# Kernel tuning notes

Measured on AMD Instinct MI355X. Metric: run time of the kernel, lower is better.

## Reference

```python
import jax, jax.numpy as jnp
import numpy as np

NUM_HEADS = 8
GRAPH_DIM = 64
K_RATIO = 0.1
SIM_THRESH = 0.6


def _gat_layer(h_in, mask, W, a_src, a_dst, b):
    # PyG GATConv (heads=1, eval mode): lin (no bias), alpha = LeakyReLU(a_src.h_j + a_dst.h_i),
    # softmax over source nodes j per target i (edges given by dense mask, self loops included), + bias.
    h = h_in @ W                                   # [N, F]
    asrc = h @ a_src                               # [N] source term
    adst = h @ a_dst                               # [N] target term
    logits = jax.nn.leaky_relu(adst[:, None] + asrc[None, :], 0.2)  # [target i, source j]
    logits = jnp.where(mask.T, logits, -1e30)      # mask[j,i]: edge src j -> dst i (symmetric here)
    alpha = jax.nn.softmax(logits, axis=-1)
    return alpha @ h + b


def _forward(x, w_qkv, w_proj, b_proj, gat0_W, gat0_asrc, gat0_adst, gat0_b,
             gat1_W, gat1_asrc, gat1_adst, gat1_b, w_g2a, b_g2a):
    B, C, H, W = x.shape
    HW = H * W
    nh = NUM_HEADS
    hd = C // nh
    scale = hd ** -0.5
    x_seq = x.reshape(B, C, HW).transpose(0, 2, 1)                 # [B, HW, C]

    # ---- build_spatial_graph ----
    importance = jnp.var(x_seq, axis=-1, ddof=1)                   # torch.var default unbiased
    N = int(HW * K_RATIO)                                          # 102 nodes
    _, top_idx = jax.lax.top_k(importance, N)                      # [B, N]
    feats = jnp.take_along_axis(x_seq, top_idx[..., None], axis=1) # [B, N, C]
    fn = feats / jnp.clip(jnp.linalg.norm(feats, axis=-1, keepdims=True), 1e-12)
    sim = fn @ fn.transpose(0, 2, 1)                               # [B, N, N]
    adj = sim > SIM_THRESH
    adj = adj | jnp.eye(N, dtype=bool)                             # GATConv add_self_loops

    # ---- per-batch GAT stack + graph_to_attn ----
    def per_graph(f, m):
        g = jax.nn.relu(_gat_layer(f, m, gat0_W, gat0_asrc, gat0_adst, gat0_b))
        g = jax.nn.relu(_gat_layer(g, m, gat1_W, gat1_asrc, gat1_adst, gat1_b))
        return jax.nn.sigmoid(g @ w_g2a.T + b_g2a)                 # [N, nh]
    gw = jax.vmap(per_graph)(feats, adj)                           # [B, N, nh]

    # ---- dense multi-head attention ----
    qkv = (x_seq @ w_qkv.T).reshape(B, HW, 3, nh, hd).transpose(2, 0, 3, 1, 4)
    q, k, v = qkv[0], qkv[1], qkv[2]                               # [B, nh, HW, hd]
    scores = jnp.einsum('bhqd,bhkd->bhqk', q, k) * scale           # [B, nh, HW, HW]

    # ---- graph modulation scatter (replaces the nested python loops) ----
    vals = jnp.where(adj[..., None], gw[:, :, None, :] * gw[:, None, :, :], 0.0)  # [B, N, N, nh]
    gm = jnp.zeros_like(scores)
    bidx = jnp.arange(B)[:, None, None]
    gm = gm.at[bidx, :, top_idx[:, :, None], top_idx[:, None, :]].set(vals)
    scores = scores + gm

    attn = jax.nn.softmax(scores, axis=-1)                         # dropout is identity in eval
    out = jnp.einsum('bhqk,bhkd->bhqd', attn, v).transpose(0, 2, 1, 3).reshape(B, HW, C)
    out = out @ w_proj.T + b_proj
    return out.transpose(0, 2, 1).reshape(B, C, H, W)


def setup_inputs() -> dict:
    key = jax.random.key(0)
    ks = jax.random.split(key, 16)
    dim, gd, nh = 256, GRAPH_DIM, NUM_HEADS
    B, H, W = 8, 32, 32
    s = 0.02
    return {
        'x': jax.random.normal(ks[0], (B, dim, H, W), dtype=jnp.float32),
        'w_qkv': s * jax.random.normal(ks[1], (3 * dim, dim), dtype=jnp.float32),
        'w_proj': s * jax.random.normal(ks[2], (dim, dim), dtype=jnp.float32),
        'b_proj': jnp.zeros((dim,), dtype=jnp.float32),
        'gat0_W': s * jax.random.normal(ks[3], (dim, gd), dtype=jnp.float32),
        'gat0_asrc': s * jax.random.normal(ks[4], (gd,), dtype=jnp.float32),
        'gat0_adst': s * jax.random.normal(ks[5], (gd,), dtype=jnp.float32),
        'gat0_b': jnp.zeros((gd,), dtype=jnp.float32),
        'gat1_W': s * jax.random.normal(ks[6], (gd, gd), dtype=jnp.float32),
        'gat1_asrc': s * jax.random.normal(ks[7], (gd,), dtype=jnp.float32),
        'gat1_adst': s * jax.random.normal(ks[8], (gd,), dtype=jnp.float32),
        'gat1_b': jnp.zeros((gd,), dtype=jnp.float32),
        'w_g2a': s * jax.random.normal(ks[9], (nh, gd), dtype=jnp.float32),
        'b_g2a': jnp.zeros((nh,), dtype=jnp.float32),
    }


def reference(x, w_qkv, w_proj, b_proj, gat0_W, gat0_asrc, gat0_adst, gat0_b,
              gat1_W, gat1_asrc, gat1_adst, gat1_b, w_g2a, b_g2a):
    return _forward(x, w_qkv, w_proj, b_proj, gat0_W, gat0_asrc, gat0_adst, gat0_b,
                    gat1_W, gat1_asrc, gat1_adst, gat1_b, w_g2a, b_g2a)
```

## Files before the change

kernel.cpp:

```cpp
#include <hip/hip_runtime.h>
#include <math.h>

#define NB 8
#define CDIM 256
#define HWD 1024
#define NH 8
#define HD 32
#define NN 102
#define GD 64

typedef __attribute__((ext_vector_type(8))) short bf16x8;
typedef __attribute__((ext_vector_type(4))) float f32x4;

__device__ inline short f2bf(float f) {
  union { float f; unsigned u; } v; v.f = f;
  unsigned r = v.u + 0x7fffu + ((v.u >> 16) & 1u);
  return (short)(r >> 16);
}
__device__ inline float bf2f(short s) {
  union { unsigned u; float f; } v;
  v.u = ((unsigned)(unsigned short)s) << 16;
  return v.f;
}

__global__ __launch_bounds__(256) void wsplit_k(const float* __restrict__ w_qkv,
                                                const float* __restrict__ w_proj,
                                                short* __restrict__ wqh, short* __restrict__ wql,
                                                short* __restrict__ wph, short* __restrict__ wpl) {
  int t = blockIdx.x * 256 + threadIdx.x;
  if (t < 196608) {
    float v = w_qkv[t];
    short hi = f2bf(v);
    wqh[t] = hi; wql[t] = f2bf(v - bf2f(hi));
  } else {
    int u = t - 196608;
    float v = w_proj[u];
    short hi = f2bf(v);
    wph[u] = hi; wpl[u] = f2bf(v - bf2f(hi));
  }
}

__global__ __launch_bounds__(256) void xsplit_k(const float* __restrict__ x,
                                                short* __restrict__ xth,
                                                short* __restrict__ xtl) {
  __shared__ float tile[64][65];
  int p0 = blockIdx.x * 64, c0 = blockIdx.y * 64, b = blockIdx.z;
  int t = threadIdx.x;
  {
    int g = t >> 6, p = t & 63;
#pragma unroll
    for (int i = 0; i < 16; ++i) {
      int cc = g * 16 + i;
      tile[cc][p] = x[((size_t)(b * 256 + c0 + cc)) * 1024 + p0 + p];
    }
  }
  __syncthreads();
  {
    int p = t >> 2, cs = (t & 3) * 16;
    size_t rb = ((size_t)(b * 1024 + p0 + p)) * 256 + c0 + cs;
#pragma unroll
    for (int g = 0; g < 4; ++g) {
      short4 hv, lv;
      float f0 = tile[cs + g * 4 + 0][p];
      float f1 = tile[cs + g * 4 + 1][p];
      float f2 = tile[cs + g * 4 + 2][p];
      float f3 = tile[cs + g * 4 + 3][p];
      hv.x = f2bf(f0); lv.x = f2bf(f0 - bf2f(hv.x));
      hv.y = f2bf(f1); lv.y = f2bf(f1 - bf2f(hv.y));
      hv.z = f2bf(f2); lv.z = f2bf(f2 - bf2f(hv.z));
      hv.w = f2bf(f3); lv.w = f2bf(f3 - bf2f(hv.w));
      *(short4*)(xth + rb + g * 4) = hv;
      *(short4*)(xtl + rb + g * 4) = lv;
    }
  }
}

__global__ __launch_bounds__(256) void prep_k(const float* __restrict__ g0W,
                                              const float* __restrict__ g1W,
                                              short* __restrict__ w0bT,
                                              short* __restrict__ w1bT) {
  int t = blockIdx.x * 256 + threadIdx.x;
  if (t < 16384) {
    int c = t >> 6, f = t & 63;
    w0bT[f * 256 + c] = f2bf(g0W[t]);
  } else if (t < 20480) {
    int u2 = t - 16384;
    int c = u2 >> 6, f = u2 & 63;
    w1bT[f * 64 + c] = f2bf(g1W[u2]);
  }
}

__global__ __launch_bounds__(256) void importance_k(const float* __restrict__ x,
                                                    float* __restrict__ imp) {
  __shared__ float red[8][33];
  int bp = blockIdx.x;
  int b = bp >> 5, p0 = (bp & 31) << 5;
  int t = threadIdx.x;
  int pl = t & 31, cg = t >> 5;
  const float* xp = x + (size_t)b * CDIM * HWD + p0 + pl;
  float s = 0.f;
  for (int cc = 0; cc < 32; ++cc) s += xp[(size_t)(cg * 32 + cc) * HWD];
  red[cg][pl] = s;
  __syncthreads();
  float tot = 0.f;
  for (int g = 0; g < 8; ++g) tot += red[g][pl];
  float mean = tot * (1.f / CDIM);
  __syncthreads();
  float v = 0.f;
  for (int cc = 0; cc < 32; ++cc) {
    float d = xp[(size_t)(cg * 32 + cc) * HWD] - mean;
    v += d * d;
  }
  red[cg][pl] = v;
  __syncthreads();
  if (t < 32) {
    float vv = 0.f;
    for (int g = 0; g < 8; ++g) vv += red[g][t];
    imp[b * 1024 + p0 + t] = vv * (1.f / (CDIM - 1));
  }
}

union GraphLDS {
  struct { float sv[1024]; int si[1024]; } tk;
  struct {
    short h0T[64 * 136];
    short alphaB[102 * 136];
    short gB[102 * 72];
  } m;
};

__global__ __launch_bounds__(1024) void graph_k(
    const float* __restrict__ x, const float* __restrict__ imp,
    const short* __restrict__ w0bT, const short* __restrict__ w1bT,
    const float* __restrict__ g0as, const float* __restrict__ g0ad,
    const float* __restrict__ g0b,
    const float* __restrict__ g1as, const float* __restrict__ g1ad,
    const float* __restrict__ g1b,
    const float* __restrict__ wg2a, const float* __restrict__ bg2a,
    int* __restrict__ nodeof, short* __restrict__ fnG,
    unsigned char* __restrict__ adjG, float* __restrict__ gwb) {
  __shared__ GraphLDS u;
  __shared__ ushort adjPack[NN][8];
  __shared__ float normL[NN];
  __shared__ float asrcL[NN], adstL[NN];
  __shared__ int topiL[NN];
  int b = blockIdx.x, t = threadIdx.x;
  int wv = t >> 6, lane = t & 63, quad = lane >> 4, l16 = lane & 15;

  u.tk.sv[t] = imp[b * 1024 + t];
  u.tk.si[t] = t;
  nodeof[b * 1024 + t] = -1;
  __syncthreads();
  for (int k = 2; k <= 1024; k <<= 1) {
    for (int j = k >> 1; j > 0; j >>= 1) {
      int ixj = t ^ j;
      if (ixj > t) {
        bool up = ((t & k) == 0);
        float a = u.tk.sv[t], c = u.tk.sv[ixj];
        if ((a > c) == up) {
          u.tk.sv[t] = c; u.tk.sv[ixj] = a;
          int ti = u.tk.si[t]; u.tk.si[t] = u.tk.si[ixj]; u.tk.si[ixj] = ti;
        }
      }
      __syncthreads();
    }
  }
  if (t >= 1024 - NN) {
    int n = 1023 - t;
    int idx = u.tk.si[t];
    topiL[n] = idx;
    nodeof[b * 1024 + idx] = n;
  }
  __syncthreads();

  {
    int n = t >> 3, g = t & 7;
    if (n < NN) {
      int idx = topiL[n];
      const float* xb = x + (size_t)b * CDIM * HWD + idx;
      float vbuf[32];
      float ssl = 0.f;
#pragma unroll
      for (int cc = 0; cc < 32; ++cc) {
        float v = xb[(size_t)(g * 32 + cc) * HWD];
        vbuf[cc] = v;
        ssl += v * v;
      }
      ssl += __shfl_xor(ssl, 1);
      ssl += __shfl_xor(ssl, 2);
      ssl += __shfl_xor(ssl, 4);
      float nrm = sqrtf(ssl);
      float rn = 1.f / fmaxf(nrm, 1e-12f);
      if (g == 0) normL[n] = nrm;
      short* fp = fnG + ((size_t)b * 112 + n) * 256 + g * 32;
#pragma unroll
      for (int cc = 0; cc < 32; cc += 4) {
        short4 s4 = {f2bf(vbuf[cc] * rn), f2bf(vbuf[cc + 1] * rn),
                     f2bf(vbuf[cc + 2] * rn), f2bf(vbuf[cc + 3] * rn)};
        *(short4*)(fp + cc) = s4;
      }
    }
  }
  for (int e = t; e < 64 * 34; e += 1024) {
    int f = e / 34, c = 102 + (e % 34);
    u.m.h0T[f * 136 + c] = 0;
  }
  __syncthreads();

  for (int tile = wv; tile < 49; tile += 16) {
    int I = tile / 7, J = tile % 7;
    const short* ap = fnG + ((size_t)b * 112 + I * 16 + l16) * 256 + quad * 8;
    const short* bp = fnG + ((size_t)b * 112 + J * 16 + l16) * 256 + quad * 8;
    f32x4 acc = (f32x4){0.f, 0.f, 0.f, 0.f};
#pragma unroll
    for (int kb = 0; kb < 8; ++kb)
      acc = __builtin_amdgcn_mfma_f32_16x16x32_bf16(*(const bf16x8*)(ap + kb * 32),
                                                    *(const bf16x8*)(bp + kb * 32), acc, 0, 0, 0);
#pragma unroll
    for (int r = 0; r < 4; ++r) {
      int i = I * 16 + quad * 4 + r, j = J * 16 + l16;
      bool e = (acc[r] > 0.6f) || (i == j);
      unsigned long long m = __ballot(e);
      if (l16 == 0) {
        int row = I * 16 + quad * 4 + r;
        if (row < NN) adjPack[row][J] = (ushort)((m >> (quad * 16)) & 0xFFFFull);
      }
      if (i < NN && j < NN) adjG[(size_t)b * NN * NN + i * NN + j] = e ? 1 : 0;
    }
  }
  __syncthreads();

  for (int tile = wv; tile < 28; tile += 16) {
    int mt = tile >> 2, nt = tile & 3;
    const short* ap = fnG + ((size_t)b * 112 + mt * 16 + l16) * 256 + quad * 8;
    const short* bp = w0bT + (nt * 16 + l16) * 256 + quad * 8;
    f32x4 acc = (f32x4){0.f, 0.f, 0.f, 0.f};
#pragma unroll
    for (int kb = 0; kb < 8; ++kb)
      acc = __builtin_amdgcn_mfma_f32_16x16x32_bf16(*(const bf16x8*)(ap + kb * 32),
                                                    *(const bf16x8*)(bp + kb * 32), acc, 0, 0, 0);
    int f = nt * 16 + l16;
#pragma unroll
    for (int r = 0; r < 4; ++r) {
      int node = mt * 16 + quad * 4 + r;
      if (node < NN) u.m.h0T[f * 136 + node] = f2bf(acc[r] * normL[node]);
    }
  }
  __syncthreads();

  for (int layer = 0; layer < 2; ++layer) {
    const float* avs = layer ? g1as : g0as;
    const float* avd = layer ? g1ad : g0ad;
    const float* bias = layer ? g1b : g0b;
    {
      int n = t >> 3, g = t & 7;
      if (n < NN) {
        float s1 = 0.f, s2 = 0.f;
#pragma unroll
        for (int uu = 0; uu < 8; ++uu) {
          int f = g * 8 + uu;
          float hv = bf2f(u.m.h0T[f * 136 + n]);
          s1 += hv * avs[f];
          s2 += hv * avd[f];
        }
        s1 += __shfl_xor(s1, 1); s1 += __shfl_xor(s1, 2); s1 += __shfl_xor(s1, 4);
        s2 += __shfl_xor(s2, 1); s2 += __shfl_xor(s2, 2); s2 += __shfl_xor(s2, 4);
        if (g == 0) { asrcL[n] = s1; adstL[n] = s2; }
      }
    }
    __syncthreads();
    for (int i = wv; i < NN; i += 16) {
      float zi = adstL[i];
      int j1 = 64 + lane;
      bool e0 = (adjPack[i][lane >> 4] >> (lane & 15)) & 1;
      bool e1 = (j1 < NN) && ((adjPack[i][j1 >> 4] >> (j1 & 15)) & 1);
      float p0 = 0.f, p1 = 0.f;
      if (e0) { float z = zi + asrcL[lane]; p0 = __expf(z > 0.f ? z : 0.2f * z); }
      if (e1) { float z = zi + asrcL[j1]; p1 = __expf(z > 0.f ? z : 0.2f * z); }
      float s = p0 + p1;
      s += __shfl_xor(s, 1); s += __shfl_xor(s, 2); s += __shfl_xor(s, 4);
      s += __shfl_xor(s, 8); s += __shfl_xor(s, 16); s += __shfl_xor(s, 32);
      float inv = 1.f / s;
      u.m.alphaB[i * 136 + lane] = f2bf(p0 * inv);
      u.m.alphaB[i * 136 + 64 + lane] = f2bf(p1 * inv);
    }
    __syncthreads();
    for (int tile = wv; tile < 28; tile += 16) {
      int mt = tile >> 2, nt = tile & 3;
      int ar = mt * 16 + l16; if (ar > NN - 1) ar = NN - 1;
      const short* ap = &u.m.alphaB[ar * 136 + quad * 8];
      const short* bp = &u.m.h0T[(nt * 16 + l16) * 136 + quad * 8];
      f32x4 acc = (f32x4){0.f, 0.f, 0.f, 0.f};
#pragma unroll
      for (int kb = 0; kb < 4; ++kb)
        acc = __builtin_amdgcn_mfma_f32_16x16x32_bf16(*(const bf16x8*)(ap + kb * 32),
                                                      *(const bf16x8*)(bp + kb * 32), acc, 0, 0, 0);
      int f = nt * 16 + l16;
      float bv = bias[f];
#pragma unroll
      for (int r = 0; r < 4; ++r) {
        int i = mt * 16 + quad * 4 + r;
        if (i < NN) u.m.gB[i * 72 + f] = f2bf(fmaxf(acc[r] + bv, 0.f));
      }
    }
    __syncthreads();
    if (layer == 0) {
      for (int tile = wv; tile < 28; tile += 16) {
        int mt = tile >> 2, nt = tile & 3;
        int ar = mt * 16 + l16; if (ar > NN - 1) ar = NN - 1;
        const short* ap = &u.m.gB[ar * 72 + quad * 8];
        const short* bp = w1bT + (nt * 16 + l16) * 64 + quad * 8;
        f32x4 acc = (f32x4){0.f, 0.f, 0.f, 0.f};
#pragma unroll
        for (int kb = 0; kb < 2; ++kb)
          acc = __builtin_amdgcn_mfma_f32_16x16x32_bf16(*(const bf16x8*)(ap + kb * 32),
                                                        *(const bf16x8*)(bp + kb * 32), acc, 0, 0, 0);
        int f = nt * 16 + l16;
#pragma unroll
        for (int r = 0; r < 4; ++r) {
          int node = mt * 16 + quad * 4 + r;
          if (node < NN) u.m.h0T[f * 136 + node] = f2bf(acc[r]);
        }
      }
      __syncthreads();
    }
  }
  float* wgL = (float*)&u.m.alphaB[0];
  if (t < 512) wgL[t] = wg2a[t];
  __syncthreads();
  if (t < NN * NH) {
    int n = t >> 3, h = t & 7;
    float z = bg2a[h];
#pragma unroll
    for (int c = 0; c < GD; ++c) z += bf2f(u.m.gB[n * 72 + c]) * wgL[h * 64 + c];
    gwb[((size_t)b * NN + n) * NH + h] = 1.f / (1.f + __expf(-z));
  }
}

__global__ __launch_bounds__(256, 4) void qkv_k(const short* __restrict__ xth,
                                                const short* __restrict__ xtl,
                                                const short* __restrict__ wqh,
                                                const short* __restrict__ wql,
                                                short* __restrict__ qhp, short* __restrict__ qlp,
                                                short* __restrict__ khp, short* __restrict__ klp,
                                                short* __restrict__ vtp) {
  __shared__ short vs_s[4][32 * 24];
  int t = threadIdx.x, wid = t >> 6, lane = t & 63, quad = lane >> 4, l16 = lane & 15;
  int m0 = blockIdx.x * 64, y = blockIdx.y;
  int b = m0 >> 10;
  int row = m0 + wid * 16 + l16;
  int p_base = (m0 & 1023) + wid * 16;
  int qi = y >> 3, n0 = (y & 7) * 32;
  const short* wh = wqh + ((size_t)qi * 256 + n0) * 256;
  const short* wl = wql + ((size_t)qi * 256 + n0) * 256;
  const short* arh = xth + (size_t)row * 256 + quad * 8;
  const short* arl = xtl + (size_t)row * 256 + quad * 8;
  f32x4 acc[2];
  acc[0] = (f32x4){0.f, 0.f, 0.f, 0.f};
  acc[1] = (f32x4){0.f, 0.f, 0.f, 0.f};
#pragma unroll
  for (int kb = 0; kb < 8; ++kb) {
    bf16x8 ah = *(const bf16x8*)(arh + kb * 32);
    bf16x8 al = *(const bf16x8*)(arl + kb * 32);
#pragma unroll
    for (int nt = 0; nt < 2; ++nt) {
      size_t wo = (size_t)(nt * 16 + l16) * 256 + kb * 32 + quad * 8;
      bf16x8 bh_ = *(const bf16x8*)(wh + wo);
      bf16x8 bl_ = *(const bf16x8*)(wl + wo);
      acc[nt] = __builtin_amdgcn_mfma_f32_16x16x32_bf16(ah, bh_, acc[nt], 0, 0, 0);
      acc[nt] = __builtin_amdgcn_mfma_f32_16x16x32_bf16(ah, bl_, acc[nt], 0, 0, 0);
      acc[nt] = __builtin_amdgcn_mfma_f32_16x16x32_bf16(al, bh_, acc[nt], 0, 0, 0);
    }
  }
  if (qi < 2) {
    const float scale = (qi == 0) ? 0.17677669529663687f : 1.f;
    short* hp = (qi == 0) ? qhp : khp;
    short* lp = (qi == 0) ? qlp : klp;
#pragma unroll
    for (int nt = 0; nt < 2; ++nt) {
      int nq = n0 + nt * 16 + l16;
      int h = nq >> 5, d = nq & 31;
#pragma unroll
      for (int r = 0; r < 4; ++r) {
        int p = p_base + quad * 4 + r;
        float v = acc[nt][r] * scale;
        short hi = f2bf(v);
        short lo = f2bf(v - bf2f(hi));
        size_t e = ((size_t)(b * 8 + h) * 1024 + p) * 32 + d;
        hp[e] = hi;
        lp[e] = lo;
      }
    }
  } else {
    short* vs = &vs_s[wid][0];
#pragma unroll
    for (int nt = 0; nt < 2; ++nt)
#pragma unroll
      for (int r = 0; r < 4; ++r)
        vs[(nt * 16 + l16) * 24 + quad * 4 + r] = f2bf(acc[nt][r]);
    int cl = lane >> 1, hf = lane & 1;
    int nq = n0 + cl;
    int h = nq >> 5, d = nq & 31;
    size_t rb = ((size_t)(b * 8 + h) * 32 + d) * 1024 + p_base + hf * 8;
    *(bf16x8*)(vtp + rb) = *(const bf16x8*)(vs + cl * 24 + hf * 8);
  }
}

__global__ __launch_bounds__(256, 4) void attn_k(const short* __restrict__ qh,
                                                 const short* __restrict__ ql,
                                                 const short* __restrict__ kh,
                                                 const short* __restrict__ kl,
                                                 const short* __restrict__ vt,
                                                 const int* __restrict__ nodeof,
                                                 const float* __restrict__ gw,
                                                 const unsigned char* __restrict__ adj,
                                                 float* __restrict__ po,
                                                 float* __restrict__ pl) {
  __shared__ __align__(16) short p_s[4][16 * 72];
  __shared__ float aw_s[4][16];
  int t = threadIdx.x;
  int wid = t >> 6, lane = t & 63, quad = lane >> 4, l16 = lane & 15;
  int bh = blockIdx.x, b = bh >> 3, h = bh & 7;
  int qt = blockIdx.y, khalf = blockIdx.z;
  int q0 = qt * 64 + wid * 16;
  size_t base = (size_t)bh * 32768;
  short* pw = &p_s[wid][0];
  float* aw = &aw_s[wid][0];

  size_t qoff = base + (size_t)(q0 + l16) * 32 + quad * 8;
  bf16x8 qhf = *(const bf16x8*)(qh + qoff);
  bf16x8 qlf = *(const bf16x8*)(ql + qoff);

  int irow[4]; float grq[4];
#pragma unroll
  for (int r = 0; r < 4; ++r) {
    int qr = q0 + quad * 4 + r;
    int in_ = nodeof[b * 1024 + qr];
    irow[r] = in_;
    grq[r] = (in_ >= 0) ? gw[((size_t)b * NN + in_) * NH + h] : 0.f;
  }
  const unsigned char* adjB = adj + (size_t)b * NN * NN;

  f32x4 ot[2];
  ot[0] = (f32x4){0.f, 0.f, 0.f, 0.f};
  ot[1] = (f32x4){0.f, 0.f, 0.f, 0.f};
  float l_r[4] = {0.f, 0.f, 0.f, 0.f};

  for (int ch = khalf * 8; ch < khalf * 8 + 8; ++ch) {
    int c0 = ch * 64;
    bf16x8 khf[4], klf[4];
#pragma unroll
    for (int ni = 0; ni < 4; ++ni) {
      size_t off = base + (size_t)(c0 + ni * 16 + l16) * 32 + quad * 8;
      khf[ni] = *(const bf16x8*)(kh + off);
      klf[ni] = *(const bf16x8*)(kl + off);
    }
    bf16x8 vaf[2][2];
#pragma unroll
    for (int mi = 0; mi < 2; ++mi)
#pragma unroll
      for (int ks = 0; ks < 2; ++ks)
        vaf[mi][ks] = *(const bf16x8*)(vt + base + (size_t)(mi * 16 + l16) * 1024 +
                                       c0 + ks * 32 + quad * 8);
    int jn[4]; float gcn[4];
#pragma unroll
    for (int ni = 0; ni < 4; ++ni) {
      int j = nodeof[b * 1024 + c0 + ni * 16 + l16];
      jn[ni] = j;
      gcn[ni] = (j >= 0) ? gw[((size_t)b * NN + j) * NH + h] : 0.f;
    }
    f32x4 s[4];
#pragma unroll
    for (int ni = 0; ni < 4; ++ni) {
      f32x4 a = (f32x4){0.f, 0.f, 0.f, 0.f};
      a = __builtin_amdgcn_mfma_f32_16x16x32_bf16(qhf, khf[ni], a, 0, 0, 0);
      a = __builtin_amdgcn_mfma_f32_16x16x32_bf16(qhf, klf[ni], a, 0, 0, 0);
      a = __builtin_amdgcn_mfma_f32_16x16x32_bf16(qlf, khf[ni], a, 0, 0, 0);
      s[ni] = a;
    }
#pragma unroll
    for (int r = 0; r < 4; ++r) {
      int in_ = irow[r];
      if (in_ >= 0) {
        const unsigned char* ar = adjB + (size_t)in_ * NN;
        float g = grq[r];
#pragma unroll
        for (int ni = 0; ni < 4; ++ni)
          if (jn[ni] >= 0 && ar[jn[ni]]) s[ni][r] += g * gcn[ni];
      }
    }
#pragma unroll
    for (int r = 0; r < 4; ++r) {
      float e0 = __expf(s[0][r]);
      float e1 = __expf(s[1][r]);
      float e2 = __expf(s[2][r]);
      float e3 = __expf(s[3][r]);
      l_r[r] += (e0 + e1) + (e2 + e3);
      int prow = (quad * 4 + r) * 72;
      pw[prow + 0 + l16] = f2bf(e0);
      pw[prow + 16 + l16] = f2bf(e1);
      pw[prow + 32 + l16] = f2bf(e2);
      pw[prow + 48 + l16] = f2bf(e3);
    }
#pragma unroll
    for (int ks = 0; ks < 2; ++ks) {
      bf16x8 pb = *(const bf16x8*)(pw + l16 * 72 + ks * 32 + quad * 8);
      ot[0] = __builtin_amdgcn_mfma_f32_16x16x32_bf16(vaf[0][ks], pb, ot[0], 0, 0, 0);
      ot[1] = __builtin_amdgcn_mfma_f32_16x16x32_bf16(vaf[1][ks], pb, ot[1], 0, 0, 0);
    }
  }
#pragma unroll
  for (int r = 0; r < 4; ++r) {
    float ls = l_r[r];
    ls += __shfl_xor(ls, 1);
    ls += __shfl_xor(ls, 2);
    ls += __shfl_xor(ls, 4);
    ls += __shfl_xor(ls, 8);
    if (l16 == 0) aw[quad * 4 + r] = ls;
  }
  float* os = (float*)pw;
#pragma unroll
  for (int mi = 0; mi < 2; ++mi)
#pragma unroll
    for (int r = 0; r < 4; ++r)
      os[l16 * 36 + mi * 16 + quad * 4 + r] = ot[mi][r];
  int bht = bh * 16 + qt;
  size_t pob = (((size_t)bht * 2 + khalf) * 64 + wid * 16) * 32;
  int qr2 = lane >> 2, dg = (lane & 3) * 8;
  *(float4*)&po[pob + qr2 * 32 + dg] = *(float4*)&os[qr2 * 36 + dg];
  *(float4*)&po[pob + qr2 * 32 + dg + 4] = *(float4*)&os[qr2 * 36 + dg + 4];
  if (lane < 16) pl[((size_t)bht * 2 + khalf) * 64 + wid * 16 + lane] = aw[lane];
}

__global__ __launch_bounds__(256) void reduce_k(const float* __restrict__ po,
                                                const float* __restrict__ pl,
                                                short* __restrict__ aoh,
                                                short* __restrict__ aol) {
  int bht = blockIdx.x;
  int bh = bht >> 4, qt = bht & 15;
  int b = bh >> 3, h = bh & 7;
  int t = threadIdx.x;
  int q = t >> 2, dg = (t & 3) * 8;
  size_t b0 = (((size_t)bht * 2 + 0) * 64 + q) * 32 + dg;
  size_t b1 = (((size_t)bht * 2 + 1) * 64 + q) * 32 + dg;
  float4 a0 = *(const float4*)&po[b0];
  float4 a1 = *(const float4*)&po[b0 + 4];
  float4 c0 = *(const float4*)&po[b1];
  float4 c1 = *(const float4*)&po[b1 + 4];
  float l = pl[((size_t)bht * 2) * 64 + q] + pl[((size_t)bht * 2 + 1) * 64 + q];
  float inv = 1.f / l;
  float f[8] = {(a0.x + c0.x) * inv, (a0.y + c0.y) * inv,
                (a0.z + c0.z) * inv, (a0.w + c0.w) * inv,
                (a1.x + c1.x) * inv, (a1.y + c1.y) * inv,
                (a1.z + c1.z) * inv, (a1.w + c1.w) * inv};
  bf16x8 hv, lv;
#pragma unroll
  for (int j = 0; j < 8; ++j) {
    hv[j] = f2bf(f[j]);
    lv[j] = f2bf(f[j] - bf2f(hv[j]));
  }
  size_t ob = (size_t)(b * 1024 + qt * 64 + q) * 256 + h * 32 + dg;
  *(bf16x8*)(aoh + ob) = hv;
  *(bf16x8*)(aol + ob) = lv;
}

__global__ __launch_bounds__(256, 4) void proj_k(const short* __restrict__ aoh,
                                                 const short* __restrict__ aol,
                                                 const short* __restrict__ wph,
                                                 const short* __restrict__ wpl,
                                                 const float* __restrict__ bias,
                                                 float* __restrict__ out) {
  __shared__ float os_s[4][32 * 20];
  int t = threadIdx.x, wid = t >> 6, lane = t & 63, quad = lane >> 4, l16 = lane & 15;
  int m0 = blockIdx.x * 64, n0 = blockIdx.y * 32;
  int b = m0 >> 10;
  int row = m0 + wid * 16 + l16;
  int p_base = (m0 & 1023) + wid * 16;
  const short* arh = aoh + (size_t)row * 256 + quad * 8;
  const short* arl = aol + (size_t)row * 256 + quad * 8;
  f32x4 acc[2];
  acc[0] = (f32x4){0.f, 0.f, 0.f, 0.f};
  acc[1] = (f32x4){0.f, 0.f, 0.f, 0.f};
#pragma unroll
  for (int kb = 0; kb < 8; ++kb) {
    bf16x8 ah = *(const bf16x8*)(arh + kb * 32);
    bf16x8 al = *(const bf16x8*)(arl + kb * 32);
#pragma unroll
    for (int nt = 0; nt < 2; ++nt) {
      size_t wo = (size_t)(n0 + nt * 16 + l16) * 256 + kb * 32 + quad * 8;
      bf16x8 bh_ = *(const bf16x8*)(wph + wo);
      bf16x8 bl_ = *(const bf16x8*)(wpl + wo);
      acc[nt] = __builtin_amdgcn_mfma_f32_16x16x32_bf16(ah, bh_, acc[nt], 0, 0, 0);
      acc[nt] = __builtin_amdgcn_mfma_f32_16x16x32_bf16(ah, bl_, acc[nt], 0, 0, 0);
      acc[nt] = __builtin_amdgcn_mfma_f32_16x16x32_bf16(al, bh_, acc[nt], 0, 0, 0);
    }
  }
  float* os = &os_s[wid][0];
#pragma unroll
  for (int nt = 0; nt < 2; ++nt) {
    float bv = bias[n0 + nt * 16 + l16];
#pragma unroll
    for (int r = 0; r < 4; ++r)
      os[(nt * 16 + l16) * 20 + quad * 4 + r] = acc[nt][r] + bv;
  }
  int cl = lane >> 1, hf = lane & 1;
  int c = n0 + cl;
  float* orow = out + ((size_t)(b * 256 + c)) * 1024 + p_base;
  *(float4*)(orow + hf * 8) = *(float4*)&os[cl * 20 + hf * 8];
  *(float4*)(orow + hf * 8 + 4) = *(float4*)&os[cl * 20 + hf * 8 + 4];
}

extern "C" void kernel_launch(void* const* d_in, const int* in_sizes, int n_in,
                              void* d_out, int out_size, void* d_ws, size_t ws_size,
                              hipStream_t stream) {
  const float* x      = (const float*)d_in[0];
  const float* w_qkv  = (const float*)d_in[1];
  const float* w_proj = (const float*)d_in[2];
  const float* b_proj = (const float*)d_in[3];
  const float* g0W    = (const float*)d_in[4];
  const float* g0as   = (const float*)d_in[5];
  const float* g0ad   = (const float*)d_in[6];
  const float* g0b    = (const float*)d_in[7];
  const float* g1W    = (const float*)d_in[8];
  const float* g1as   = (const float*)d_in[9];
  const float* g1ad   = (const float*)d_in[10];
  const float* g1b    = (const float*)d_in[11];
  const float* wg2a   = (const float*)d_in[12];
  const float* bg2a   = (const float*)d_in[13];
  float* out = (float*)d_out;
  float* ws = (float*)d_ws;

  size_t o = 0;
  auto alloc = [&](size_t nf) { float* p = ws + o; o += (nf + 15) & ~(size_t)15; return p; };
  float* imp    = alloc(8 * 1024);
  int*   nodeof = (int*)alloc(8 * 1024);
  short* fnG    = (short*)alloc(8 * 112 * 256 / 2);
  short* w0bT   = (short*)alloc(256 * 64 / 2);
  short* w1bT   = (short*)alloc(64 * 64 / 2);
  unsigned char* adj = (unsigned char*)alloc((8 * NN * NN + 3) / 4 + 16);
  float* gwb    = alloc(8 * NN * 8);
  short* xth    = (short*)alloc(1048576);
  short* xtl    = (short*)alloc(1048576);
  short* wqh    = (short*)alloc(98304);
  short* wql    = (short*)alloc(98304);
  short* wph    = (short*)alloc(32768);
  short* wpl    = (short*)alloc(32768);
  short* qh     = (short*)alloc(1048576);
  short* ql     = (short*)alloc(1048576);
  short* kh     = (short*)alloc(1048576);
  short* kl     = (short*)alloc(1048576);
  short* vt     = (short*)alloc(1048576);
  short* aoh    = (short*)alloc(1048576);
  short* aol    = (short*)alloc(1048576);
  float* po     = alloc((size_t)1024 * 2 * 64 * 32);
  float* plv    = alloc((size_t)1024 * 2 * 64);
  if (ws_size < o * sizeof(float)) return;

  importance_k<<<256, 256, 0, stream>>>(x, imp);
  wsplit_k<<<1024, 256, 0, stream>>>(w_qkv, w_proj, wqh, wql, wph, wpl);
  xsplit_k<<<dim3(16, 4, 8), 256, 0, stream>>>(x, xth, xtl);
  prep_k<<<80, 256, 0, stream>>>(g0W, g1W, w0bT, w1bT);
  graph_k<<<8, 1024, 0, stream>>>(x, imp, w0bT, w1bT, g0as, g0ad, g0b,
                                  g1as, g1ad, g1b, wg2a, bg2a,
                                  nodeof, fnG, adj, gwb);
  qkv_k<<<dim3(128, 24), 256, 0, stream>>>(xth, xtl, wqh, wql, qh, ql, kh, kl, vt);
  attn_k<<<dim3(64, 16, 2), 256, 0, stream>>>(qh, ql, kh, kl, vt, nodeof, gwb, adj, po, plv);
  reduce_k<<<1024, 256, 0, stream>>>(po, plv, aoh, aol);
  proj_k<<<dim3(128, 8), 256, 0, stream>>>(aoh, aol, wph, wpl, b_proj, out);
}
```

Baseline: 369.1 us.

## Precompute position-space adjacency bitmasks and per-head graph weights for attention

New measurement: 365.8 us. About the same (-0.9%).

```diff
diff --git a/kernel.cpp b/kernel.cpp
--- a/kernel.cpp
+++ b/kernel.cpp
@@ -137,7 +137,7 @@
     const float* __restrict__ g1as, const float* __restrict__ g1ad,
     const float* __restrict__ g1b,
     const float* __restrict__ wg2a, const float* __restrict__ bg2a,
-    int* __restrict__ nodeof, short* __restrict__ fnG,
+    int* __restrict__ nodeof, int* __restrict__ topi, short* __restrict__ fnG,
     unsigned char* __restrict__ adjG, float* __restrict__ gwb) {
   __shared__ GraphLDS u;
   __shared__ ushort adjPack[NN][8];
@@ -169,6 +169,7 @@
     int n = 1023 - t;
     int idx = u.tk.si[t];
     topiL[n] = idx;
+    topi[b * 128 + n] = idx;
     nodeof[b * 1024 + idx] = n;
   }
   __syncthreads();
@@ -335,6 +336,35 @@
     for (int c = 0; c < GD; ++c) z += bf2f(u.m.gB[n * 72 + c]) * wgL[h * 64 + c];
     gwb[((size_t)b * NN + n) * NH + h] = 1.f / (1.f + __expf(-z));
   }
+}
+
+__global__ __launch_bounds__(128) void posadj_k(const int* __restrict__ nodeof,
+                                                const int* __restrict__ topi,
+                                                const unsigned char* __restrict__ adjG,
+                                                const float* __restrict__ gwb,
+                                                unsigned long long* __restrict__ posadj,
+                                                float* __restrict__ gwp) {
+  int b = blockIdx.y, p = blockIdx.x * 128 + threadIdx.x;
+  int n = nodeof[b * 1024 + p];
+#pragma unroll
+  for (int h = 0; h < 8; ++h)
+    gwp[(size_t)(b * 8 + h) * 1024 + p] =
+        (n >= 0) ? gwb[((size_t)b * NN + n) * NH + h] : 0.f;
+  unsigned long long m[16];
+#pragma unroll
+  for (int w = 0; w < 16; ++w) m[w] = 0;
+  if (n >= 0) {
+    const unsigned char* ar = adjG + (size_t)b * NN * NN + (size_t)n * NN;
+    for (int nj = 0; nj < NN; ++nj) {
+      if (ar[nj]) {
+        int pj = topi[b * 128 + nj];
+        m[pj >> 6] |= 1ull << (pj & 63);
+      }
+    }
+  }
+  unsigned long long* dst = posadj + (size_t)(b * 1024 + p) * 16;
+#pragma unroll
+  for (int w = 0; w < 16; ++w) dst[w] = m[w];
 }
 
 __global__ __launch_bounds__(256, 4) void qkv_k(const short* __restrict__ xth,
@@ -411,16 +441,15 @@
                                                  const short* __restrict__ kh,
                                                  const short* __restrict__ kl,
                                                  const short* __restrict__ vt,
-                                                 const int* __restrict__ nodeof,
-                                                 const float* __restrict__ gw,
-                                                 const unsigned char* __restrict__ adj,
+                                                 const float* __restrict__ gwp,
+                                                 const unsigned long long* __restrict__ posadj,
                                                  float* __restrict__ po,
                                                  float* __restrict__ pl) {
   __shared__ __align__(16) short p_s[4][16 * 72];
   __shared__ float aw_s[4][16];
   int t = threadIdx.x;
   int wid = t >> 6, lane = t & 63, quad = lane >> 4, l16 = lane & 15;
-  int bh = blockIdx.x, b = bh >> 3, h = bh & 7;
+  int bh = blockIdx.x, b = bh >> 3;
   int qt = blockIdx.y, khalf = blockIdx.z;
   int q0 = qt * 64 + wid * 16;
   size_t base = (size_t)bh * 32768;
@@ -431,15 +460,11 @@
   bf16x8 qhf = *(const bf16x8*)(qh + qoff);
   bf16x8 qlf = *(const bf16x8*)(ql + qoff);
 
-  int irow[4]; float grq[4];
-#pragma unroll
-  for (int r = 0; r < 4; ++r) {
-    int qr = q0 + quad * 4 + r;
-    int in_ = nodeof[b * 1024 + qr];
-    irow[r] = in_;
-    grq[r] = (in_ >= 0) ? gw[((size_t)b * NN + in_) * NH + h] : 0.f;
-  }
-  const unsigned char* adjB = adj + (size_t)b * NN * NN;
+  const float* gwpBH = gwp + (size_t)bh * 1024;
+  const unsigned long long* paB = posadj + (size_t)b * 1024 * 16;
+  float grq[4];
+#pragma unroll
+  for (int r = 0; r < 4; ++r) grq[r] = gwpBH[q0 + quad * 4 + r];
 
   f32x4 ot[2];
   ot[0] = (f32x4){0.f, 0.f, 0.f, 0.f};
@@ -462,13 +487,13 @@
       for (int ks = 0; ks < 2; ++ks)
         vaf[mi][ks] = *(const bf16x8*)(vt + base + (size_t)(mi * 16 + l16) * 1024 +
                                        c0 + ks * 32 + quad * 8);
-    int jn[4]; float gcn[4];
-#pragma unroll
-    for (int ni = 0; ni < 4; ++ni) {
-      int j = nodeof[b * 1024 + c0 + ni * 16 + l16];
-      jn[ni] = j;
-      gcn[ni] = (j >= 0) ? gw[((size_t)b * NN + j) * NH + h] : 0.f;
-    }
+    float gc[4];
+#pragma unroll
+    for (int ni = 0; ni < 4; ++ni) gc[ni] = gwpBH[c0 + ni * 16 + l16];
+    unsigned long long mr[4];
+#pragma unroll
+    for (int r = 0; r < 4; ++r)
+      mr[r] = paB[(size_t)(q0 + quad * 4 + r) * 16 + ch];
     f32x4 s[4];
 #pragma unroll
     for (int ni = 0; ni < 4; ++ni) {
@@ -480,13 +505,10 @@
     }
 #pragma unroll
     for (int r = 0; r < 4; ++r) {
-      int in_ = irow[r];
-      if (in_ >= 0) {
-        const unsigned char* ar = adjB + (size_t)in_ * NN;
-        float g = grq[r];
-#pragma unroll
-        for (int ni = 0; ni < 4; ++ni)
-          if (jn[ni] >= 0 && ar[jn[ni]]) s[ni][r] += g * gcn[ni];
+#pragma unroll
+      for (int ni = 0; ni < 4; ++ni) {
+        bool bit = (mr[r] >> (ni * 16 + l16)) & 1ull;
+        s[ni][r] += bit ? grq[r] * gc[ni] : 0.f;
       }
     }
 #pragma unroll
@@ -634,11 +656,14 @@
   auto alloc = [&](size_t nf) { float* p = ws + o; o += (nf + 15) & ~(size_t)15; return p; };
   float* imp    = alloc(8 * 1024);
   int*   nodeof = (int*)alloc(8 * 1024);
+  int*   topi   = (int*)alloc(8 * 128);
   short* fnG    = (short*)alloc(8 * 112 * 256 / 2);
   short* w0bT   = (short*)alloc(256 * 64 / 2);
   short* w1bT   = (short*)alloc(64 * 64 / 2);
   unsigned char* adj = (unsigned char*)alloc((8 * NN * NN + 3) / 4 + 16);
   float* gwb    = alloc(8 * NN * 8);
+  unsigned long long* posadj = (unsigned long long*)alloc(8 * 1024 * 16 * 2);
+  float* gwp    = alloc(64 * 1024);
   short* xth    = (short*)alloc(1048576);
   short* xtl    = (short*)alloc(1048576);
   short* wqh    = (short*)alloc(98304);
@@ -662,9 +687,10 @@
   prep_k<<<80, 256, 0, stream>>>(g0W, g1W, w0bT, w1bT);
   graph_k<<<8, 1024, 0, stream>>>(x, imp, w0bT, w1bT, g0as, g0ad, g0b,
                                   g1as, g1ad, g1b, wg2a, bg2a,
-                                  nodeof, fnG, adj, gwb);
+                                  nodeof, topi, fnG, adj, gwb);
+  posadj_k<<<dim3(8, 8), 128, 0, stream>>>(nodeof, topi, adj, gwb, posadj, gwp);
   qkv_k<<<dim3(128, 24), 256, 0, stream>>>(xth, xtl, wqh, wql, qh, ql, kh, kl, vt);
-  attn_k<<<dim3(64, 16, 2), 256, 0, stream>>>(qh, ql, kh, kl, vt, nodeof, gwb, adj, po, plv);
+  attn_k<<<dim3(64, 16, 2), 256, 0, stream>>>(qh, ql, kh, kl, vt, gwp, posadj, po, plv);
   reduce_k<<<1024, 256, 0, stream>>>(po, plv, aoh, aol);
   proj_k<<<dim3(128, 8), 256, 0, stream>>>(aoh, aol, wph, wpl, b_proj, out);
 }
```
